# Kernel optimization log

Hardware: AMD Instinct MI355X
Metric: run time of the kernel (lower is better)

Reference implementation:

```python
import jax, jax.numpy as jnp
import numpy as np

B, S, D = 8, 2048, 1024      # batch, seq (tokens), in/out token dim
E = 2 * D                    # expansion dim (expansion_factor=2)
SDIM = 128                   # attention feature dim s
SQRT_S = float(np.sqrt(SDIM))
EPS_LN = 1e-5                # ScaleNorm eps


def setup_inputs() -> dict:
    key = jax.random.key(0)
    ks = jax.random.split(key, 8)
    return {
        "x": jax.random.normal(ks[0], (B, S, D), jnp.float32),
        "pos_enc": jax.random.normal(ks[1], (S, SDIM), jnp.float32),
        "ln_g": jnp.ones((1,), jnp.float32),                                   # ScaleNorm scalar gain
        "uv_w": jax.random.normal(ks[2], (2 * E + SDIM, D), jnp.float32) / np.sqrt(D),  # fused uv proj (xavier-ish)
        "gamma": jax.random.uniform(ks[3], (2, SDIM), jnp.float32),            # q/k affine scale
        "beta": jax.random.uniform(ks[4], (2, SDIM), jnp.float32),             # q/k affine shift
        "o_w": jax.random.normal(ks[5], (D, E), jnp.float32) / np.sqrt(E),     # output proj
        "res_scale": jnp.ones((D,), jnp.float32),                              # ChannelWiseScale
    }


def reference(x, pos_enc, ln_g, uv_w, gamma, beta, o_w, res_scale):
    # ScaleNorm: x / clamp(||x|| * d^-0.5, eps) * g
    norm = jnp.linalg.norm(x, axis=-1, keepdims=True) * (D ** -0.5)
    xn = x / jnp.maximum(norm, EPS_LN) * ln_g
    # fused uv projection + SiLU
    uv = jax.nn.silu(xn @ uv_w.T)                      # [B,S,2E+s]
    u = uv[..., :E]                                    # gate
    v = uv[..., E:2 * E]                               # values
    base = uv[..., 2 * E:]                             # shared q/k base [B,S,s]
    qk_base = base[..., None, :] * gamma + beta        # [B,S,2,s]
    q = qk_base[..., 0, :] + pos_enc                   # add positional enc [B,S,s]
    k = qk_base[..., 1, :] + pos_enc
    # squared-ReLU attention kernel
    kernel = jnp.square(jax.nn.relu(jnp.einsum('bqs,bks->bqk', q, k) / SQRT_S))
    out = (u * jnp.einsum('bqk,bke->bqe', kernel, v)) @ o_w.T  # [B,S,D]
    # channel-wise scaled residual (in_dims == out_dims -> shortcut)
    return x * res_scale + out
```

## Files before the change

kernel.cpp:

```cpp
#include <hip/hip_runtime.h>
#include <stdint.h>

#define B_   8
#define S_   2048
#define D_   1024
#define E_   2048
#define SD_  128
#define M_   (B_ * S_)
#define NUV  (2 * E_ + SD_)
#define NUV2 4352

typedef __attribute__((ext_vector_type(8))) short short8;
typedef __attribute__((ext_vector_type(4))) float floatx4;

typedef __attribute__((address_space(1))) void as1_void;
typedef __attribute__((address_space(3))) void as3_void;

__device__ __forceinline__ ushort f2bf(float f) {
    uint32_t u = __float_as_uint(f);
    uint32_t r = (u + 0x7fffu + ((u >> 16) & 1u)) >> 16;
    return (ushort)r;
}
__device__ __forceinline__ float bf2f(ushort h) {
    return __uint_as_float(((uint32_t)h) << 16);
}
__device__ __forceinline__ float silu(float z) {
    return z * __builtin_amdgcn_rcpf(1.0f + __expf(-z));
}
__device__ __forceinline__ void gld_lds16(const ushort* g, ushort* l) {
    __builtin_amdgcn_global_load_lds((const as1_void*)g, (as3_void*)l, 16, 0, 0);
}


__device__ __forceinline__ void tile_swizzle(int& mt, int& nt) {
    const int gx  = gridDim.x;
    const int lin = blockIdx.y * gx + blockIdx.x;
    const int bandSz = gx * 8;
    const int band = lin / bandSz;
    const int rem  = lin - band * bandSz;
    const int full = gx >> 2;
    const int sc   = rem >> 5;
    if (sc < full) {
        const int r2 = rem & 31;
        mt = band * 8 + (r2 & 7);
        nt = sc * 4 + (r2 >> 3);
    } else {
        const int r3 = rem - full * 32;
        mt = band * 8 + (r3 & 7);
        nt = full * 4 + (r3 >> 3);
    }
}

__device__ __forceinline__ void gemm_core(
    const ushort* __restrict__ A, const ushort* __restrict__ B,
    int lda, int ldb, int K, int m0, int n0,
    ushort* ldsA, ushort* ldsB, floatx4 acc[4][4])
{
    const int t    = threadIdx.x;
    const int lane = t & 63;
    const int l15  = lane & 15;
    const int quad = lane >> 4;
    const int wave = t >> 6;
    const int wm   = (wave >> 1) * 64;
    const int wn   = (wave & 1) * 64;
    const int key  = l15 & 7;

    const ushort* gA[4]; const ushort* gB[4];
    ushort* lA[4]; ushort* lB[4];
    #pragma unroll
    for (int i = 0; i < 4; ++i) {
        const int c   = t + i * 256;
        const int row = c >> 3;
        const int gkc = ((c & 7) ^ (row & 7)) * 8;
        gA[i] = A + (size_t)(m0 + row) * lda + gkc;
        gB[i] = B + (size_t)(n0 + row) * ldb + gkc;
        lA[i] = ldsA + c * 8;
        lB[i] = ldsB + c * 8;
    }

    for (int kk = 0; kk < K; kk += 64) {
        __syncthreads();
        #pragma unroll
        for (int i = 0; i < 4; ++i) gld_lds16(gA[i] + kk, lA[i]);
        #pragma unroll
        for (int i = 0; i < 4; ++i) gld_lds16(gB[i] + kk, lB[i]);
        __syncthreads();

        #pragma unroll
        for (int s = 0; s < 2; ++s) {
            const int koff = ((s * 4 + quad) ^ key) * 8;
            short8 af[4], bfr[4];
            #pragma unroll
            for (int mi = 0; mi < 4; ++mi)
                af[mi] = *(const short8*)(ldsA + (wm + mi * 16 + l15) * 64 + koff);
            #pragma unroll
            for (int ni = 0; ni < 4; ++ni)
                bfr[ni] = *(const short8*)(ldsB + (wn + ni * 16 + l15) * 64 + koff);
            #pragma unroll
            for (int mi = 0; mi < 4; ++mi)
                #pragma unroll
                for (int ni = 0; ni < 4; ++ni)
                    acc[mi][ni] = __builtin_amdgcn_mfma_f32_16x16x32_bf16(
                        af[mi], bfr[ni], acc[mi][ni], 0, 0, 0);
        }
    }
}

#define EPI_INDICES \
    const int t = threadIdx.x; \
    const int lane = t & 63, l15 = lane & 15, quad = lane >> 4; \
    const int wave = t >> 6, wm = (wave >> 1) * 64, wn = (wave & 1) * 64; \
    (void)t;

#define ZERO_ACC \
    floatx4 acc[4][4]; \
    _Pragma("unroll") \
    for (int i = 0; i < 4; ++i) \
        _Pragma("unroll") \
        for (int j = 0; j < 4; ++j) \
            _Pragma("unroll") \
            for (int r = 0; r < 4; ++r) acc[i][j][r] = 0.0f;


__device__ __forceinline__ void tile_swizzle4(int& mt, int& nt) {
    const int gx  = gridDim.x;
    const int lin = blockIdx.y * gx + blockIdx.x;
    const int bandSz = gx * 4;
    const int band = lin / bandSz;
    const int rem  = lin - band * bandSz;
    const int full = gx >> 2;
    const int sc   = rem >> 4;
    if (sc < full) {
        const int r2 = rem & 15;
        mt = band * 4 + (r2 & 3);
        nt = sc * 4 + (r2 >> 2);
    } else {
        const int r3 = rem - full * 16;
        mt = band * 4 + (r3 & 3);
        nt = full * 4 + (r3 >> 2);
    }
}

#define STAGE_A(bufn, h, kk) { \
    gld_lds16(gA0 + (size_t)(h) * a128 + (kk), LA##bufn + (h) * 8192 + t * 8); \
    gld_lds16(gA1 + (size_t)(h) * a128 + (kk), LA##bufn + (h) * 8192 + t * 8 + 4096); }
#define STAGE_B(bufn, h, kk) { \
    gld_lds16(gB0 + (size_t)(h) * b128 + (kk), LB##bufn + (h) * 8192 + t * 8); \
    gld_lds16(gB1 + (size_t)(h) * b128 + (kk), LB##bufn + (h) * 8192 + t * 8 + 4096); }

#define PHA(bufn, STAGES) { \
    short8 af_[4][2]; \
    { const ushort* pa_ = LA##bufn + aoff; \
      const ushort* pb_ = LB##bufn + boff; \
      _Pragma("unroll") \
      for (int mi_ = 0; mi_ < 4; ++mi_) { \
          af_[mi_][0] = *(const short8*)(pa_ + mi_ * 1024 + koff0); \
          af_[mi_][1] = *(const short8*)(pa_ + mi_ * 1024 + koff1); } \
      _Pragma("unroll") \
      for (int nq_ = 0; nq_ < 2; ++nq_) \
      _Pragma("unroll") \
      for (int ni_ = 0; ni_ < 2; ++ni_) { \
          bfv[nq_][ni_][0] = *(const short8*)(pb_ + nq_ * 8192 + ni_ * 1024 + koff0); \
          bfv[nq_][ni_][1] = *(const short8*)(pb_ + nq_ * 8192 + ni_ * 1024 + koff1); } } \
    STAGES \
    __builtin_amdgcn_s_barrier(); \
    asm volatile("s_waitcnt lgkmcnt(0)" ::: "memory"); \
    __builtin_amdgcn_sched_barrier(0); \
    __builtin_amdgcn_s_setprio(1); \
    _Pragma("unroll") \
    for (int nq_ = 0; nq_ < 2; ++nq_) \
    _Pragma("unroll") \
    for (int mi_ = 0; mi_ < 4; ++mi_) \
    _Pragma("unroll") \
    for (int ni_ = 0; ni_ < 2; ++ni_) { \
        acc[0][nq_][mi_][ni_] = __builtin_amdgcn_mfma_f32_16x16x32_bf16( \
            af_[mi_][0], bfv[nq_][ni_][0], acc[0][nq_][mi_][ni_], 0, 0, 0); \
        acc[0][nq_][mi_][ni_] = __builtin_amdgcn_mfma_f32_16x16x32_bf16( \
            af_[mi_][1], bfv[nq_][ni_][1], acc[0][nq_][mi_][ni_], 0, 0, 0); } \
    __builtin_amdgcn_s_setprio(0); \
    __builtin_amdgcn_s_barrier(); }

#define PHB(bufn, STAGES, WAITC) { \
    short8 af_[4][2]; \
    { const ushort* pa_ = LA##bufn + 8192 + aoff; \
      _Pragma("unroll") \
      for (int mi_ = 0; mi_ < 4; ++mi_) { \
          af_[mi_][0] = *(const short8*)(pa_ + mi_ * 1024 + koff0); \
          af_[mi_][1] = *(const short8*)(pa_ + mi_ * 1024 + koff1); } } \
    STAGES \
    __builtin_amdgcn_s_barrier(); \
    asm volatile("s_waitcnt lgkmcnt(0)" ::: "memory"); \
    __builtin_amdgcn_sched_barrier(0); \
    __builtin_amdgcn_s_setprio(1); \
    _Pragma("unroll") \
    for (int nq_ = 0; nq_ < 2; ++nq_) \
    _Pragma("unroll") \
    for (int mi_ = 0; mi_ < 4; ++mi_) \
    _Pragma("unroll") \
    for (int ni_ = 0; ni_ < 2; ++ni_) { \
        acc[1][nq_][mi_][ni_] = __builtin_amdgcn_mfma_f32_16x16x32_bf16( \
            af_[mi_][0], bfv[nq_][ni_][0], acc[1][nq_][mi_][ni_], 0, 0, 0); \
        acc[1][nq_][mi_][ni_] = __builtin_amdgcn_mfma_f32_16x16x32_bf16( \
            af_[mi_][1], bfv[nq_][ni_][1], acc[1][nq_][mi_][ni_], 0, 0, 0); } \
    __builtin_amdgcn_s_setprio(0); \
    WAITC \
    __builtin_amdgcn_s_barrier(); }

__device__ __forceinline__ void gemm256(
    const ushort* __restrict__ A, const ushort* __restrict__ B,
    int lda, int ldb, int K, int m0, int n0,
    ushort* lds, floatx4 (&acc)[2][2][4][2])
{
    const int t    = threadIdx.x;
    const int lane = t & 63;
    const int l15  = lane & 15;
    const int quad = lane >> 4;
    const int w    = t >> 6;
    const int wr   = w >> 2;
    const int wc   = w & 3;
    const int key  = l15 & 7;
    const int aoff  = (wr * 64 + l15) * 64;
    const int boff  = (wc * 32 + l15) * 64;
    const int koff0 = (quad ^ key) * 8;
    const int koff1 = ((quad + 4) ^ key) * 8;

    ushort* const LA0 = lds;
    ushort* const LA1 = lds + 16384;
    ushort* const LB0 = lds + 32768;
    ushort* const LB1 = lds + 49152;

    const int r0 = t >> 3;
    const int k0 = ((t & 7) ^ (r0 & 7)) * 8;
    const ushort* gA0 = A + (size_t)(m0 + r0) * lda + k0;
    const ushort* gA1 = gA0 + (size_t)64 * lda;
    const ushort* gB0 = B + (size_t)(n0 + r0) * ldb + k0;
    const ushort* gB1 = gB0 + (size_t)64 * ldb;
    const size_t a128 = (size_t)128 * lda;
    const size_t b128 = (size_t)128 * ldb;

    short8 bfv[2][2][2];

    STAGE_A(0, 0, 0) STAGE_A(0, 1, 0) STAGE_B(0, 0, 0) STAGE_B(0, 1, 0)
    STAGE_A(1, 0, 64) STAGE_B(1, 0, 64) STAGE_B(1, 1, 64)
    asm volatile("s_waitcnt vmcnt(6)" ::: "memory");
    __builtin_amdgcn_s_barrier();

    const int nIter = K >> 7;
    #pragma unroll 1
    for (int i = 0; i < nIter; ++i) {
        const bool lastI = (i == nIter - 1);
        const int kb = i * 128;
        PHA(0, STAGE_A(1, 1, kb + 64))
        PHB(0, if (!lastI) { STAGE_A(0, 0, kb + 128) STAGE_B(0, 0, kb + 128) STAGE_B(0, 1, kb + 128) },
               if (!lastI) { asm volatile("s_waitcnt vmcnt(6)" ::: "memory"); }
               else        { asm volatile("s_waitcnt vmcnt(0)" ::: "memory"); })
        PHA(1, if (!lastI) { STAGE_A(0, 1, kb + 128) })
        PHB(1, if (!lastI) { STAGE_A(1, 0, kb + 192) STAGE_B(1, 0, kb + 192) STAGE_B(1, 1, kb + 192) },
               if (!lastI) { asm volatile("s_waitcnt vmcnt(6)" ::: "memory"); })
    }
}

#define ZERO_ACC256 \
    floatx4 acc[2][2][4][2]; \
    _Pragma("unroll") for (int zq_ = 0; zq_ < 2; ++zq_) \
    _Pragma("unroll") for (int zn_ = 0; zn_ < 2; ++zn_) \
    _Pragma("unroll") for (int zm_ = 0; zm_ < 4; ++zm_) \
    _Pragma("unroll") for (int zl_ = 0; zl_ < 2; ++zl_) \
    _Pragma("unroll") for (int zr_ = 0; zr_ < 4; ++zr_) \
        acc[zq_][zn_][zm_][zl_][zr_] = 0.0f;

#define EPI256 \
    const int t = threadIdx.x; \
    const int lane = t & 63, l15 = lane & 15, quad = lane >> 4; \
    const int w = t >> 6, wr = w >> 2, wc = w & 3; \
    (void)t; (void)lane;

__global__ __launch_bounds__(256) void k_cvt(const float* __restrict__ src,
                                             ushort* __restrict__ dst, int n4) {
    int i = blockIdx.x * 256 + threadIdx.x;
    if (i < n4) {
        float4 v = ((const float4*)src)[i];
        ushort4 o;
        o.x = f2bf(v.x); o.y = f2bf(v.y); o.z = f2bf(v.z); o.w = f2bf(v.w);
        ((ushort4*)dst)[i] = o;
    }
}

__global__ __launch_bounds__(256) void k_rmsnorm(const float* __restrict__ x,
                                                 const float* __restrict__ ln_g,
                                                 ushort* __restrict__ xnb) {
    const int m = blockIdx.x;
    const int t = threadIdx.x;
    float4 v = ((const float4*)(x + (size_t)m * D_))[t];
    float ss = v.x * v.x + v.y * v.y + v.z * v.z + v.w * v.w;
    #pragma unroll
    for (int off = 32; off > 0; off >>= 1) ss += __shfl_down(ss, off, 64);
    __shared__ float red[4];
    if ((t & 63) == 0) red[t >> 6] = ss;
    __syncthreads();
    float tot = red[0] + red[1] + red[2] + red[3];
    float rms = sqrtf(tot * (1.0f / (float)D_));
    float scale = ln_g[0] / fmaxf(rms, 1e-5f);
    ushort4 o;
    o.x = f2bf(v.x * scale); o.y = f2bf(v.y * scale);
    o.z = f2bf(v.z * scale); o.w = f2bf(v.w * scale);
    ((ushort4*)(xnb + (size_t)m * D_))[t] = o;
}

__global__ __launch_bounds__(256, 3) void k_gemm1(
    const ushort* __restrict__ xnb, const ushort* __restrict__ uvwb,
    const float* __restrict__ gamma, const float* __restrict__ beta,
    const float* __restrict__ pos,
    ushort* __restrict__ u, ushort* __restrict__ vT,
    ushort* __restrict__ qb, ushort* __restrict__ kb)
{
    __shared__ __align__(16) ushort lds[17408];
    ushort* ldsA = lds;
    ushort* ldsB = lds + 8192;
    ZERO_ACC
    int mt, nt;
    tile_swizzle(mt, nt);
    const int m0 = mt * 128;
    const int n0 = nt * 128;
    gemm_core(xnb, uvwb, D_, D_, D_, m0, n0, ldsA, ldsB, acc);
    EPI_INDICES

    if (nt < 16) {
        #pragma unroll
        for (int mi = 0; mi < 4; ++mi)
            #pragma unroll
            for (int ni = 0; ni < 4; ++ni) {
                const int col = n0 + wn + ni * 16 + l15;
                #pragma unroll
                for (int r = 0; r < 4; ++r) {
                    const int row = m0 + wm + mi * 16 + quad * 4 + r;
                    u[(size_t)row * E_ + col] = f2bf(silu(acc[mi][ni][r]));
                }
            }
    } else if (nt < 32) {
        const int b   = m0 >> 11;
        const int s0  = m0 & (S_ - 1);
        const int ec0 = n0 - E_;
        __syncthreads();
        #pragma unroll
        for (int mi = 0; mi < 4; ++mi)
            #pragma unroll
            for (int ni = 0; ni < 4; ++ni) {
                const int col = wn + ni * 16 + l15;
                const int row = wm + mi * 16 + quad * 4;
                #pragma unroll
                for (int r = 0; r < 4; r += 2) {
                    ushort2 pr;
                    pr.x = f2bf(silu(acc[mi][ni][r]));
                    pr.y = f2bf(silu(acc[mi][ni][r + 1]));
                    *(ushort2*)&lds[col * 136 + row + r] = pr;
                }
            }
        __syncthreads();
        ushort* vTb = vT + ((size_t)b * E_ + ec0) * S_ + s0;
        #pragma unroll
        for (int i = 0; i < 8; ++i) {
            const int lin = i * 256 + t;
            const int e  = lin >> 4;
            const int sb = (lin & 15) * 8;
            *(short8*)(vTb + (size_t)e * S_ + sb) = *(const short8*)&lds[e * 136 + sb];
        }
    } else {
        #pragma unroll
        for (int mi = 0; mi < 4; ++mi)
            #pragma unroll
            for (int ni = 0; ni < 4; ++ni) {
                const int sd = wn + ni * 16 + l15;
                const float g0 = gamma[sd], g1 = gamma[SD_ + sd];
                const float be0 = beta[sd], be1 = beta[SD_ + sd];
                #pragma unroll
                for (int r = 0; r < 4; ++r) {
                    const int row = m0 + wm + mi * 16 + quad * 4 + r;
                    const int srow = row & (S_ - 1);
                    float s = silu(acc[mi][ni][r]);
                    const float p = pos[(size_t)srow * SD_ + sd];
                    qb[(size_t)row * SD_ + sd] = f2bf(s * g0 + be0 + p);
                    kb[(size_t)row * SD_ + sd] = f2bf(s * g1 + be1 + p);
                }
            }
    }
}

__global__ __launch_bounds__(512, 2) void k_scores(
    const ushort* __restrict__ qb, const ushort* __restrict__ kb,
    ushort* __restrict__ kern, int b_off)
{
    __shared__ __align__(16) ushort lds[65536];
    ZERO_ACC256
    const int bz = blockIdx.z;
    const int b  = b_off + bz;
    int mt, nt;
    tile_swizzle4(mt, nt);
    const int m0 = mt * 256, n0 = nt * 256;
    gemm256(qb + (size_t)b * S_ * SD_, kb + (size_t)b * S_ * SD_,
            SD_, SD_, SD_, m0, n0, lds, acc);
    EPI256
    ushort* ko = kern + (size_t)bz * S_ * S_;
    const float inv = 0.08838834764831845f;
    #pragma unroll
    for (int mq = 0; mq < 2; ++mq)
    #pragma unroll
    for (int nq = 0; nq < 2; ++nq)
    #pragma unroll
    for (int mi = 0; mi < 4; ++mi)
    #pragma unroll
    for (int ni = 0; ni < 2; ++ni) {
        const int col = n0 + nq * 128 + wc * 32 + ni * 16 + l15;
        const int rb  = m0 + mq * 128 + wr * 64 + mi * 16 + quad * 4;
        #pragma unroll
        for (int r = 0; r < 4; ++r) {
            float s = fmaxf(acc[mq][nq][mi][ni][r] * inv, 0.0f);
            ko[(size_t)(rb + r) * S_ + col] = f2bf(s * s);
        }
    }
}

__global__ __launch_bounds__(512, 2) void k_kv(
    const ushort* __restrict__ kern, const ushort* __restrict__ vT,
    const ushort* __restrict__ u, ushort* __restrict__ kvu, int b_off)
{
    __shared__ __align__(16) ushort lds[65536];
    ZERO_ACC256
    const int bz = blockIdx.z;
    const int b  = b_off + bz;
    int mt, nt;
    tile_swizzle4(mt, nt);
    const int m0 = mt * 256, n0 = nt * 256;
    gemm256(kern + (size_t)bz * S_ * S_, vT + (size_t)b * E_ * S_,
            S_, S_, S_, m0, n0, lds, acc);
    EPI256
    #pragma unroll
    for (int mq = 0; mq < 2; ++mq)
    #pragma unroll
    for (int nq = 0; nq < 2; ++nq)
    #pragma unroll
    for (int mi = 0; mi < 4; ++mi)
    #pragma unroll
    for (int ni = 0; ni < 2; ++ni) {
        const int col = n0 + nq * 128 + wc * 32 + ni * 16 + l15;
        const int rb  = m0 + mq * 128 + wr * 64 + mi * 16 + quad * 4;
        #pragma unroll
        for (int r = 0; r < 4; ++r) {
            const size_t gi = (size_t)(b * S_ + rb + r) * E_ + col;
            float uval = bf2f(u[gi]);
            kvu[gi] = f2bf(uval * acc[mq][nq][mi][ni][r]);
        }
    }
}

__global__ __launch_bounds__(512, 2) void k_out(
    const ushort* __restrict__ kvu, const ushort* __restrict__ owb,
    const float* __restrict__ x, const float* __restrict__ res_scale,
    float* __restrict__ out)
{
    __shared__ __align__(16) ushort lds[65536];
    ZERO_ACC256
    int mt, nt;
    tile_swizzle4(mt, nt);
    const int m0 = mt * 256, n0 = nt * 256;
    gemm256(kvu, owb, E_, E_, E_, m0, n0, lds, acc);
    EPI256
    #pragma unroll
    for (int mq = 0; mq < 2; ++mq)
    #pragma unroll
    for (int nq = 0; nq < 2; ++nq)
    #pragma unroll
    for (int mi = 0; mi < 4; ++mi)
    #pragma unroll
    for (int ni = 0; ni < 2; ++ni) {
        const int col = n0 + nq * 128 + wc * 32 + ni * 16 + l15;
        const float rs = res_scale[col];
        const int rb = m0 + mq * 128 + wr * 64 + mi * 16 + quad * 4;
        #pragma unroll
        for (int r = 0; r < 4; ++r) {
            const size_t gi = (size_t)(rb + r) * D_ + col;
            out[gi] = x[gi] * rs + acc[mq][nq][mi][ni][r];
        }
    }
}

extern "C" void kernel_launch(void* const* d_in, const int* in_sizes, int n_in,
                              void* d_out, int out_size, void* d_ws, size_t ws_size,
                              hipStream_t stream)
{
    const float* x         = (const float*)d_in[0];
    const float* pos       = (const float*)d_in[1];
    const float* ln_g      = (const float*)d_in[2];
    const float* uv_w      = (const float*)d_in[3];
    const float* gamma     = (const float*)d_in[4];
    const float* beta      = (const float*)d_in[5];
    const float* o_w       = (const float*)d_in[6];
    const float* res_scale = (const float*)d_in[7];
    float* out = (float*)d_out;

    char* p = (char*)d_ws;
    ushort* region0 = (ushort*)p; p += (size_t)M_ * D_ * 2;
    ushort* uvwb    = (ushort*)p; p += (size_t)NUV2 * D_ * 2;
    ushort* owb     = (ushort*)p; p += (size_t)D_ * E_ * 2;
    ushort* u       = (ushort*)p; p += (size_t)M_ * E_ * 2;
    ushort* kvu     = (ushort*)p; p += (size_t)M_ * E_ * 2;
    ushort* vT      = (ushort*)p; p += (size_t)M_ * E_ * 2;
    ushort* qb      = (ushort*)p; p += (size_t)M_ * SD_ * 2;
    ushort* kb      = (ushort*)p; p += (size_t)M_ * SD_ * 2;

    ushort* xnb  = region0;
    ushort* kern = region0;

    k_cvt<<<(NUV * D_ / 4 + 255) / 256, 256, 0, stream>>>(uv_w, uvwb, NUV * D_ / 4);
    k_cvt<<<(D_ * E_ / 4 + 255) / 256, 256, 0, stream>>>(o_w, owb, D_ * E_ / 4);
    k_rmsnorm<<<M_, 256, 0, stream>>>(x, ln_g, xnb);
    k_gemm1<<<dim3(NUV / 128, M_ / 128), 256, 0, stream>>>(xnb, uvwb, gamma, beta, pos, u, vT, qb, kb);
    for (int g = 0; g < 2; ++g) {
        k_scores<<<dim3(S_ / 256, S_ / 256, 4), 512, 0, stream>>>(qb, kb, kern, g * 4);
        k_kv<<<dim3(E_ / 256, S_ / 256, 4), 512, 0, stream>>>(kern, vT, u, kvu, g * 4);
    }
    k_out<<<dim3(D_ / 256, M_ / 256), 512, 0, stream>>>(kvu, owb, x, res_scale, out);
}
```

Baseline: 548.1 us.

## Preload both A halves in PHA and move k_scores to 128-tile GEMM core

```diff
diff --git a/kernel.cpp b/kernel.cpp
--- a/kernel.cpp
+++ b/kernel.cpp
@@ -150,12 +150,17 @@
 
 #define PHA(bufn, STAGES) { \
     short8 af_[4][2]; \
-    { const ushort* pa_ = LA##bufn + aoff; \
-      const ushort* pb_ = LB##bufn + boff; \
+    { const ushort* pa_  = LA##bufn + aoff; \
+      const ushort* pa1_ = LA##bufn + 8192 + aoff; \
+      const ushort* pb_  = LB##bufn + boff; \
       _Pragma("unroll") \
       for (int mi_ = 0; mi_ < 4; ++mi_) { \
           af_[mi_][0] = *(const short8*)(pa_ + mi_ * 1024 + koff0); \
           af_[mi_][1] = *(const short8*)(pa_ + mi_ * 1024 + koff1); } \
+      _Pragma("unroll") \
+      for (int mi_ = 0; mi_ < 4; ++mi_) { \
+          afB[mi_][0] = *(const short8*)(pa1_ + mi_ * 1024 + koff0); \
+          afB[mi_][1] = *(const short8*)(pa1_ + mi_ * 1024 + koff1); } \
       _Pragma("unroll") \
       for (int nq_ = 0; nq_ < 2; ++nq_) \
       _Pragma("unroll") \
@@ -180,17 +185,9 @@
     __builtin_amdgcn_s_setprio(0); \
     __builtin_amdgcn_s_barrier(); }
 
-#define PHB(bufn, STAGES, WAITC) { \
-    short8 af_[4][2]; \
-    { const ushort* pa_ = LA##bufn + 8192 + aoff; \
-      _Pragma("unroll") \
-      for (int mi_ = 0; mi_ < 4; ++mi_) { \
-          af_[mi_][0] = *(const short8*)(pa_ + mi_ * 1024 + koff0); \
-          af_[mi_][1] = *(const short8*)(pa_ + mi_ * 1024 + koff1); } } \
+#define PHB(STAGES, WAITC) { \
     STAGES \
     __builtin_amdgcn_s_barrier(); \
-    asm volatile("s_waitcnt lgkmcnt(0)" ::: "memory"); \
-    __builtin_amdgcn_sched_barrier(0); \
     __builtin_amdgcn_s_setprio(1); \
     _Pragma("unroll") \
     for (int nq_ = 0; nq_ < 2; ++nq_) \
@@ -199,9 +196,9 @@
     _Pragma("unroll") \
     for (int ni_ = 0; ni_ < 2; ++ni_) { \
         acc[1][nq_][mi_][ni_] = __builtin_amdgcn_mfma_f32_16x16x32_bf16( \
-            af_[mi_][0], bfv[nq_][ni_][0], acc[1][nq_][mi_][ni_], 0, 0, 0); \
+            afB[mi_][0], bfv[nq_][ni_][0], acc[1][nq_][mi_][ni_], 0, 0, 0); \
         acc[1][nq_][mi_][ni_] = __builtin_amdgcn_mfma_f32_16x16x32_bf16( \
-            af_[mi_][1], bfv[nq_][ni_][1], acc[1][nq_][mi_][ni_], 0, 0, 0); } \
+            afB[mi_][1], bfv[nq_][ni_][1], acc[1][nq_][mi_][ni_], 0, 0, 0); } \
     __builtin_amdgcn_s_setprio(0); \
     WAITC \
     __builtin_amdgcn_s_barrier(); }
@@ -239,6 +236,7 @@
     const size_t b128 = (size_t)128 * ldb;
 
     short8 bfv[2][2][2];
+    short8 afB[4][2];
 
     STAGE_A(0, 0, 0) STAGE_A(0, 1, 0) STAGE_B(0, 0, 0) STAGE_B(0, 1, 0)
     STAGE_A(1, 0, 64) STAGE_B(1, 0, 64) STAGE_B(1, 1, 64)
@@ -251,12 +249,12 @@
         const bool lastI = (i == nIter - 1);
         const int kb = i * 128;
         PHA(0, STAGE_A(1, 1, kb + 64))
-        PHB(0, if (!lastI) { STAGE_A(0, 0, kb + 128) STAGE_B(0, 0, kb + 128) STAGE_B(0, 1, kb + 128) },
-               if (!lastI) { asm volatile("s_waitcnt vmcnt(6)" ::: "memory"); }
-               else        { asm volatile("s_waitcnt vmcnt(0)" ::: "memory"); })
+        PHB(if (!lastI) { STAGE_A(0, 0, kb + 128) STAGE_B(0, 0, kb + 128) STAGE_B(0, 1, kb + 128) },
+            if (!lastI) { asm volatile("s_waitcnt vmcnt(6)" ::: "memory"); }
+            else        { asm volatile("s_waitcnt vmcnt(0)" ::: "memory"); })
         PHA(1, if (!lastI) { STAGE_A(0, 1, kb + 128) })
-        PHB(1, if (!lastI) { STAGE_A(1, 0, kb + 192) STAGE_B(1, 0, kb + 192) STAGE_B(1, 1, kb + 192) },
-               if (!lastI) { asm volatile("s_waitcnt vmcnt(6)" ::: "memory"); })
+        PHB(if (!lastI) { STAGE_A(1, 0, kb + 192) STAGE_B(1, 0, kb + 192) STAGE_B(1, 1, kb + 192) },
+            if (!lastI) { asm volatile("s_waitcnt vmcnt(6)" ::: "memory"); })
     }
 }
 
@@ -386,38 +384,36 @@
     }
 }
 
-__global__ __launch_bounds__(512, 2) void k_scores(
+__global__ __launch_bounds__(256, 3) void k_scores(
     const ushort* __restrict__ qb, const ushort* __restrict__ kb,
     ushort* __restrict__ kern, int b_off)
 {
-    __shared__ __align__(16) ushort lds[65536];
-    ZERO_ACC256
+    __shared__ __align__(16) ushort ldsA[128 * 64];
+    __shared__ __align__(16) ushort ldsB[128 * 64];
+    ZERO_ACC
     const int bz = blockIdx.z;
     const int b  = b_off + bz;
     int mt, nt;
-    tile_swizzle4(mt, nt);
-    const int m0 = mt * 256, n0 = nt * 256;
-    gemm256(qb + (size_t)b * S_ * SD_, kb + (size_t)b * S_ * SD_,
-            SD_, SD_, SD_, m0, n0, lds, acc);
-    EPI256
+    tile_swizzle(mt, nt);
+    const int m0 = mt * 128;
+    const int n0 = nt * 128;
+    gemm_core(qb + (size_t)b * S_ * SD_, kb + (size_t)b * S_ * SD_,
+              SD_, SD_, SD_, m0, n0, ldsA, ldsB, acc);
+    EPI_INDICES
     ushort* ko = kern + (size_t)bz * S_ * S_;
     const float inv = 0.08838834764831845f;
     #pragma unroll
-    for (int mq = 0; mq < 2; ++mq)
-    #pragma unroll
-    for (int nq = 0; nq < 2; ++nq)
-    #pragma unroll
     for (int mi = 0; mi < 4; ++mi)
-    #pragma unroll
-    for (int ni = 0; ni < 2; ++ni) {
-        const int col = n0 + nq * 128 + wc * 32 + ni * 16 + l15;
-        const int rb  = m0 + mq * 128 + wr * 64 + mi * 16 + quad * 4;
-        #pragma unroll
-        for (int r = 0; r < 4; ++r) {
-            float s = fmaxf(acc[mq][nq][mi][ni][r] * inv, 0.0f);
-            ko[(size_t)(rb + r) * S_ + col] = f2bf(s * s);
+        #pragma unroll
+        for (int ni = 0; ni < 4; ++ni) {
+            const int col = n0 + wn + ni * 16 + l15;
+            #pragma unroll
+            for (int r = 0; r < 4; ++r) {
+                const int row = m0 + wm + mi * 16 + quad * 4 + r;
+                float s = fmaxf(acc[mi][ni][r] * inv, 0.0f);
+                ko[(size_t)row * S_ + col] = f2bf(s * s);
+            }
         }
-    }
 }
 
 __global__ __launch_bounds__(512, 2) void k_kv(
@@ -516,7 +512,7 @@
     k_rmsnorm<<<M_, 256, 0, stream>>>(x, ln_g, xnb);
     k_gemm1<<<dim3(NUV / 128, M_ / 128), 256, 0, stream>>>(xnb, uvwb, gamma, beta, pos, u, vT, qb, kb);
     for (int g = 0; g < 2; ++g) {
-        k_scores<<<dim3(S_ / 256, S_ / 256, 4), 512, 0, stream>>>(qb, kb, kern, g * 4);
+        k_scores<<<dim3(S_ / 128, S_ / 128, 4), 256, 0, stream>>>(qb, kb, kern, g * 4);
         k_kv<<<dim3(E_ / 256, S_ / 256, 4), 512, 0, stream>>>(kern, vT, u, kvu, g * 4);
     }
     k_out<<<dim3(D_ / 256, M_ / 256), 512, 0, stream>>>(kvu, owb, x, res_scale, out);
```

Result: slower. 559.8 us (+2.1%).
